# Performance work log

Measured on AMD Instinct MI355X. Metric: run time of the kernel, lower is better.

## Reference

```python
import jax, jax.numpy as jnp
import numpy as np

POOL_SIZE = 4
MAX_DIM = 256
GRID = MAX_DIM // POOL_SIZE  # 64
N_VOX = GRID ** 3            # 262144
N = 1_000_000
C = 64


def setup_inputs() -> dict:
    key = jax.random.key(0)
    k1, k2 = jax.random.split(key)
    vertices = jax.random.randint(k1, (N, 3), 0, MAX_DIM, dtype=jnp.int64)
    features = jax.random.normal(k2, (N, C), dtype=jnp.float32)
    return {"vertices": vertices, "features": features}


def reference(vertices, features):
    # floor-divide coords into voxel grid
    v = vertices // POOL_SIZE                      # [N,3] in [0, GRID)
    vox = v[:, 0] * (GRID * GRID) + v[:, 1] * GRID + v[:, 2]  # [N] flat voxel id
    # amax-pool features per voxel (empty voxels get -inf identity)
    pooled = jax.ops.segment_max(features, vox, num_segments=N_VOX)  # [N_VOX, C]
    # voxels with no points must be 0 (torch output_features initialized to zeros)
    counts = jax.ops.segment_sum(jnp.ones((vertices.shape[0],), jnp.int32), vox,
                                 num_segments=N_VOX)
    out = jnp.where((counts > 0)[:, None], pooled, jnp.zeros((), features.dtype))
    return out.reshape(-1)  # [N_VOX * C]
```

## Files before the change

kernel.cpp:

```cpp
#include <hip/hip_runtime.h>

#define GRID 64
#define N_VOX (GRID * GRID * GRID)
#define NCH 64
#define NCHUNK 256


typedef float f32x4 __attribute__((ext_vector_type(4)));
typedef int   i32x4 __attribute__((ext_vector_type(4)));

__device__ __forceinline__ int vox_of(int x, int y, int z) {
    return ((x >> 2) << 12) | ((y >> 2) << 6) | (z >> 2);
}

__device__ __forceinline__ float4 max4(float4 a, float4 b) {
    float4 r;
    r.x = fmaxf(a.x, b.x); r.y = fmaxf(a.y, b.y);
    r.z = fmaxf(a.z, b.z); r.w = fmaxf(a.w, b.w);
    return r;
}

__device__ __forceinline__ float4 ntload4(const float4* p) {
    f32x4 v = __builtin_nontemporal_load((const f32x4*)p);
    return make_float4(v[0], v[1], v[2], v[3]);
}
__device__ __forceinline__ void ntstore4(float4* p, float4 v) {
    f32x4 t; t[0] = v.x; t[1] = v.y; t[2] = v.z; t[3] = v.w;
    __builtin_nontemporal_store(t, (f32x4*)p);
}
__device__ __forceinline__ int4 ntload_i4(const int4* p) {
    i32x4 v = __builtin_nontemporal_load((const i32x4*)p);
    return make_int4(v[0], v[1], v[2], v[3]);
}

__global__ void k_hist(const int* __restrict__ verts, int* __restrict__ vox,
                       int* __restrict__ rank, int* __restrict__ counts, int n) {
    int t  = blockIdx.x * blockDim.x + threadIdx.x;
    int p0 = t * 8;
    if (p0 >= n) return;

    if (p0 + 8 <= n) {
        const int4* v4 = (const int4*)verts;
        int4 a = ntload_i4(&v4[6 * t + 0]);
        int4 b = ntload_i4(&v4[6 * t + 1]);
        int4 c = ntload_i4(&v4[6 * t + 2]);
        int4 d = ntload_i4(&v4[6 * t + 3]);
        int4 e = ntload_i4(&v4[6 * t + 4]);
        int4 f = ntload_i4(&v4[6 * t + 5]);
        int w0 = vox_of(a.x, a.y, a.z);
        int w1 = vox_of(a.w, b.x, b.y);
        int w2 = vox_of(b.z, b.w, c.x);
        int w3 = vox_of(c.y, c.z, c.w);
        int w4 = vox_of(d.x, d.y, d.z);
        int w5 = vox_of(d.w, e.x, e.y);
        int w6 = vox_of(e.z, e.w, f.x);
        int w7 = vox_of(f.y, f.z, f.w);
        ((int4*)vox)[2 * t + 0] = make_int4(w0, w1, w2, w3);
        ((int4*)vox)[2 * t + 1] = make_int4(w4, w5, w6, w7);
        int r0 = atomicAdd(&counts[w0], 1);
        int r1 = atomicAdd(&counts[w1], 1);
        int r2 = atomicAdd(&counts[w2], 1);
        int r3 = atomicAdd(&counts[w3], 1);
        int r4 = atomicAdd(&counts[w4], 1);
        int r5 = atomicAdd(&counts[w5], 1);
        int r6 = atomicAdd(&counts[w6], 1);
        int r7 = atomicAdd(&counts[w7], 1);
        ((int4*)rank)[2 * t + 0] = make_int4(r0, r1, r2, r3);
        ((int4*)rank)[2 * t + 1] = make_int4(r4, r5, r6, r7);
    } else {
        for (int p = p0; p < n; p++) {
            int w = vox_of(verts[3 * p], verts[3 * p + 1], verts[3 * p + 2]);
            vox[p]  = w;
            rank[p] = atomicAdd(&counts[w], 1);
        }
    }
}

__global__ void __launch_bounds__(256)
k_scan(const int* __restrict__ counts, int* __restrict__ gstart,
       unsigned long long* __restrict__ state, int* __restrict__ ticket) {
    __shared__ int s_ticket;
    __shared__ int wbase[4];
    __shared__ int s_base;

    if (threadIdx.x == 0) s_ticket = atomicAdd(ticket, 1);
    __syncthreads();
    const int b    = s_ticket;
    const int t    = threadIdx.x;
    const int lane = t & 63;
    const int wid  = t >> 6;

    int4 c = ((const int4*)counts)[b * 256 + t];
    int s = c.x + c.y + c.z + c.w;

    int incl = s;
    #pragma unroll
    for (int off = 1; off < 64; off <<= 1) {
        int u = __shfl_up(incl, off);
        if (lane >= off) incl += u;
    }
    if (lane == 63) wbase[wid] = incl;
    __syncthreads();

    if (wid == 0) {
        int agg = wbase[0] + wbase[1] + wbase[2] + wbase[3];
        if (lane == 0) {
            __hip_atomic_store(&state[b], (1ULL << 32) | (unsigned)agg,
                               __ATOMIC_RELEASE, __HIP_MEMORY_SCOPE_AGENT);
        }
        int excl = 0;
        int p_hi = b - 1;
        while (p_hi >= 0) {
            int p = p_hi - lane;
            unsigned long long v;
            do {
                v = (p >= 0)
                  ? __hip_atomic_load(&state[p], __ATOMIC_ACQUIRE,
                                      __HIP_MEMORY_SCOPE_AGENT)
                  : (2ULL << 32);
            } while (__any((int)((v >> 32) == 0)));
            unsigned long long m = __ballot((int)((v >> 32) == 2));
            int cut = m ? (__ffsll((long long)m) - 1) : 64;
            int contrib = (lane <= cut) ? (int)(unsigned)v : 0;
            #pragma unroll
            for (int o = 32; o; o >>= 1) contrib += __shfl_down(contrib, o);
            excl += __shfl(contrib, 0);
            if (m) break;
            p_hi -= 64;
        }
        if (lane == 0) {
            int agg2 = wbase[0] + wbase[1] + wbase[2] + wbase[3];
            __hip_atomic_store(&state[b], (2ULL << 32) | (unsigned)(excl + agg2),
                               __ATOMIC_RELEASE, __HIP_MEMORY_SCOPE_AGENT);
            s_base = excl;
            if (b == NCHUNK - 1) gstart[N_VOX] = excl + agg2;
        }
    }
    __syncthreads();

    int wexcl = 0;
    for (int i = 0; i < wid; i++) wexcl += wbase[i];
    int base = s_base + wexcl + (incl - s);
    int4 g;
    g.x = base;
    g.y = base + c.x;
    g.z = base + c.x + c.y;
    g.w = base + c.x + c.y + c.z;
    ((int4*)gstart)[b * 256 + t] = g;
}

__global__ void k_scatter_idx(const int* __restrict__ vox,
                              const int* __restrict__ rank,
                              const int* __restrict__ gstart,
                              int* __restrict__ sorted_idx, int n) {
    int t  = blockIdx.x * blockDim.x + threadIdx.x;
    int p0 = t * 8;
    if (p0 >= n) return;

    if (p0 + 8 <= n) {
        int4 w0 = ((const int4*)vox)[2 * t + 0];
        int4 w1 = ((const int4*)vox)[2 * t + 1];
        int4 r0 = ((const int4*)rank)[2 * t + 0];
        int4 r1 = ((const int4*)rank)[2 * t + 1];
        sorted_idx[gstart[w0.x] + r0.x] = p0 + 0;
        sorted_idx[gstart[w0.y] + r0.y] = p0 + 1;
        sorted_idx[gstart[w0.z] + r0.z] = p0 + 2;
        sorted_idx[gstart[w0.w] + r0.w] = p0 + 3;
        sorted_idx[gstart[w1.x] + r1.x] = p0 + 4;
        sorted_idx[gstart[w1.y] + r1.y] = p0 + 5;
        sorted_idx[gstart[w1.z] + r1.z] = p0 + 6;
        sorted_idx[gstart[w1.w] + r1.w] = p0 + 7;
    } else {
        for (int p = p0; p < n; p++)
            sorted_idx[gstart[vox[p]] + rank[p]] = p;
    }
}

#define VPB 16
#define IDX_CAP 2048

__global__ void __launch_bounds__(256)
k_gather(const int* __restrict__ sorted_idx,
         const int* __restrict__ gstart,
         const float4* __restrict__ feats4,
         float4* __restrict__ out4) {
    __shared__ int sst[VPB + 1];
    __shared__ int sidx[IDX_CAP];

    int vox0 = blockIdx.x * VPB;
    if (threadIdx.x < VPB + 1) sst[threadIdx.x] = gstart[vox0 + threadIdx.x];
    __syncthreads();

    int bstart = sst[0];
    int span   = sst[VPB] - bstart;
    bool fits  = (span <= IDX_CAP);
    if (fits) {
        for (int i = threadIdx.x; i < span; i += 256)
            sidx[i] = sorted_idx[bstart + i];
    }
    __syncthreads();

    int g   = threadIdx.x >> 4;
    int sub = threadIdx.x & 15;
    int s0  = sst[g];
    int cnt = sst[g + 1] - s0;
    float4* outp = &out4[(size_t)(vox0 + g) * 16 + sub];

    if (cnt == 0) {
        ntstore4(outp, make_float4(0.f, 0.f, 0.f, 0.f));
        return;
    }

    int off = s0 - bstart;
    float4 a0 = make_float4(-INFINITY, -INFINITY, -INFINITY, -INFINITY);
    float4 a1 = a0, a2 = a0, a3 = a0;

    int j = 0;
    for (; j + 4 <= cnt; j += 4) {
        int p0, p1, p2, p3;
        if (fits) {
            p0 = sidx[off + j];     p1 = sidx[off + j + 1];
            p2 = sidx[off + j + 2]; p3 = sidx[off + j + 3];
        } else {
            p0 = sorted_idx[s0 + j];     p1 = sorted_idx[s0 + j + 1];
            p2 = sorted_idx[s0 + j + 2]; p3 = sorted_idx[s0 + j + 3];
        }
        a0 = max4(a0, ntload4(&feats4[(size_t)p0 * 16 + sub]));
        a1 = max4(a1, ntload4(&feats4[(size_t)p1 * 16 + sub]));
        a2 = max4(a2, ntload4(&feats4[(size_t)p2 * 16 + sub]));
        a3 = max4(a3, ntload4(&feats4[(size_t)p3 * 16 + sub]));
    }
    for (; j < cnt; j++) {
        int p = fits ? sidx[off + j] : sorted_idx[s0 + j];
        a0 = max4(a0, ntload4(&feats4[(size_t)p * 16 + sub]));
    }
    ntstore4(outp, max4(max4(a0, a1), max4(a2, a3)));
}

extern "C" void kernel_launch(void* const* d_in, const int* in_sizes, int n_in,
                              void* d_out, int out_size, void* d_ws, size_t ws_size,
                              hipStream_t stream) {
    const int*   verts = (const int*)d_in[0];
    const float* feats = (const float*)d_in[1];
    float*       out   = (float*)d_out;

    const int n_pts = in_sizes[0] / 3;

    char* w = (char*)d_ws;
    int*  vox        = (int*)w;              w += (size_t)n_pts * 4;
    int*  rank       = (int*)w;              w += (size_t)n_pts * 4;
    int*  sorted_idx = (int*)w;              w += (size_t)n_pts * 4;
    int*  counts     = (int*)w;              w += (size_t)N_VOX * 4;
    unsigned long long* state = (unsigned long long*)w;  w += (size_t)NCHUNK * 8;
    int*  ticket     = (int*)w;              w += 16;
    const size_t zero_bytes = (size_t)N_VOX * 4 + (size_t)NCHUNK * 8 + 16;
    int*  gstart     = (int*)w;              w += (size_t)(N_VOX + 4) * 4;

    hipMemsetAsync(counts, 0, zero_bytes, stream);

    {
        const int block = 256;
        const int nthr  = (n_pts + 7) / 8;
        const int grid  = (nthr + block - 1) / block;
        k_hist<<<grid, block, 0, stream>>>(verts, vox, rank, counts, n_pts);
    }
    k_scan<<<NCHUNK, 256, 0, stream>>>(counts, gstart, state, ticket);

    {
        const int block = 256;
        const int nthr  = (n_pts + 7) / 8;
        const int grid  = (nthr + block - 1) / block;
        k_scatter_idx<<<grid, block, 0, stream>>>(vox, rank, gstart,
                                                  sorted_idx, n_pts);
    }
    {
        const int block = 256;
        const int grid  = N_VOX / VPB;
        k_gather<<<grid, block, 0, stream>>>(sorted_idx, gstart,
                                             (const float4*)feats, (float4*)out);
    }
}
```

Before: 433.2 us.

## Scatter features into sorted order then segment-max contiguously

Replaces the index scatter plus indirect gather with a pass that copies each point's full 256-byte feature row into voxel-sorted order, followed by a segment-max over contiguous rows. This removes the random feature reads and the sorted-index indirection from the reduction, at the cost of writing and re-reading a 256 MB intermediate buffer. The histogram kernel also drops from 8 to 4 points per thread. The scatter writes are random-position but whole-row coalesced.

```diff
diff --git a/kernel.cpp b/kernel.cpp
--- a/kernel.cpp
+++ b/kernel.cpp
@@ -36,37 +36,24 @@
 __global__ void k_hist(const int* __restrict__ verts, int* __restrict__ vox,
                        int* __restrict__ rank, int* __restrict__ counts, int n) {
     int t  = blockIdx.x * blockDim.x + threadIdx.x;
-    int p0 = t * 8;
+    int p0 = t * 4;
     if (p0 >= n) return;
 
-    if (p0 + 8 <= n) {
+    if (p0 + 4 <= n) {
         const int4* v4 = (const int4*)verts;
-        int4 a = ntload_i4(&v4[6 * t + 0]);
-        int4 b = ntload_i4(&v4[6 * t + 1]);
-        int4 c = ntload_i4(&v4[6 * t + 2]);
-        int4 d = ntload_i4(&v4[6 * t + 3]);
-        int4 e = ntload_i4(&v4[6 * t + 4]);
-        int4 f = ntload_i4(&v4[6 * t + 5]);
+        int4 a = ntload_i4(&v4[3 * t + 0]);
+        int4 b = ntload_i4(&v4[3 * t + 1]);
+        int4 c = ntload_i4(&v4[3 * t + 2]);
         int w0 = vox_of(a.x, a.y, a.z);
         int w1 = vox_of(a.w, b.x, b.y);
         int w2 = vox_of(b.z, b.w, c.x);
         int w3 = vox_of(c.y, c.z, c.w);
-        int w4 = vox_of(d.x, d.y, d.z);
-        int w5 = vox_of(d.w, e.x, e.y);
-        int w6 = vox_of(e.z, e.w, f.x);
-        int w7 = vox_of(f.y, f.z, f.w);
-        ((int4*)vox)[2 * t + 0] = make_int4(w0, w1, w2, w3);
-        ((int4*)vox)[2 * t + 1] = make_int4(w4, w5, w6, w7);
+        ((int4*)vox)[t] = make_int4(w0, w1, w2, w3);
         int r0 = atomicAdd(&counts[w0], 1);
         int r1 = atomicAdd(&counts[w1], 1);
         int r2 = atomicAdd(&counts[w2], 1);
         int r3 = atomicAdd(&counts[w3], 1);
-        int r4 = atomicAdd(&counts[w4], 1);
-        int r5 = atomicAdd(&counts[w5], 1);
-        int r6 = atomicAdd(&counts[w6], 1);
-        int r7 = atomicAdd(&counts[w7], 1);
-        ((int4*)rank)[2 * t + 0] = make_int4(r0, r1, r2, r3);
-        ((int4*)rank)[2 * t + 1] = make_int4(r4, r5, r6, r7);
+        ((int4*)rank)[t] = make_int4(r0, r1, r2, r3);
     } else {
         for (int p = p0; p < n; p++) {
             int w = vox_of(verts[3 * p], verts[3 * p + 1], verts[3 * p + 2]);
@@ -149,92 +136,52 @@
     ((int4*)gstart)[b * 256 + t] = g;
 }
 
-__global__ void k_scatter_idx(const int* __restrict__ vox,
-                              const int* __restrict__ rank,
-                              const int* __restrict__ gstart,
-                              int* __restrict__ sorted_idx, int n) {
-    int t  = blockIdx.x * blockDim.x + threadIdx.x;
-    int p0 = t * 8;
-    if (p0 >= n) return;
-
-    if (p0 + 8 <= n) {
-        int4 w0 = ((const int4*)vox)[2 * t + 0];
-        int4 w1 = ((const int4*)vox)[2 * t + 1];
-        int4 r0 = ((const int4*)rank)[2 * t + 0];
-        int4 r1 = ((const int4*)rank)[2 * t + 1];
-        sorted_idx[gstart[w0.x] + r0.x] = p0 + 0;
-        sorted_idx[gstart[w0.y] + r0.y] = p0 + 1;
-        sorted_idx[gstart[w0.z] + r0.z] = p0 + 2;
-        sorted_idx[gstart[w0.w] + r0.w] = p0 + 3;
-        sorted_idx[gstart[w1.x] + r1.x] = p0 + 4;
-        sorted_idx[gstart[w1.y] + r1.y] = p0 + 5;
-        sorted_idx[gstart[w1.z] + r1.z] = p0 + 6;
-        sorted_idx[gstart[w1.w] + r1.w] = p0 + 7;
-    } else {
-        for (int p = p0; p < n; p++)
-            sorted_idx[gstart[vox[p]] + rank[p]] = p;
-    }
-}
-
-#define VPB 16
-#define IDX_CAP 2048
-
 __global__ void __launch_bounds__(256)
-k_gather(const int* __restrict__ sorted_idx,
-         const int* __restrict__ gstart,
-         const float4* __restrict__ feats4,
-         float4* __restrict__ out4) {
-    __shared__ int sst[VPB + 1];
-    __shared__ int sidx[IDX_CAP];
-
-    int vox0 = blockIdx.x * VPB;
-    if (threadIdx.x < VPB + 1) sst[threadIdx.x] = gstart[vox0 + threadIdx.x];
-    __syncthreads();
-
-    int bstart = sst[0];
-    int span   = sst[VPB] - bstart;
-    bool fits  = (span <= IDX_CAP);
-    if (fits) {
-        for (int i = threadIdx.x; i < span; i += 256)
-            sidx[i] = sorted_idx[bstart + i];
-    }
-    __syncthreads();
-
-    int g   = threadIdx.x >> 4;
-    int sub = threadIdx.x & 15;
-    int s0  = sst[g];
-    int cnt = sst[g + 1] - s0;
-    float4* outp = &out4[(size_t)(vox0 + g) * 16 + sub];
-
-    if (cnt == 0) {
-        ntstore4(outp, make_float4(0.f, 0.f, 0.f, 0.f));
-        return;
-    }
-
-    int off = s0 - bstart;
+k_scatter_feat(const int* __restrict__ vox, const int* __restrict__ rank,
+               const int* __restrict__ gstart,
+               const float4* __restrict__ feats4,
+               float4* __restrict__ sfeat4, int n) {
+    int t   = blockIdx.x * 256 + threadIdx.x;
+    int grp = t >> 4;
+    int sub = t & 15;
+    int gw  = grp & ~3;
+    int gl  = grp & 3;
+    int pbase = gw * 4 + gl;
+
+    #pragma unroll
+    for (int i = 0; i < 4; i++) {
+        int p = pbase + i * 4;
+        if (p >= n) break;
+        float4 f = ntload4(&feats4[(size_t)p * 16 + sub]);
+        int dst = gstart[vox[p]] + rank[p];
+        sfeat4[(size_t)dst * 16 + sub] = f;
+    }
+}
+
+__global__ void __launch_bounds__(256)
+k_seg_max(const int* __restrict__ gstart,
+          const float4* __restrict__ sfeat4,
+          float4* __restrict__ out4) {
+    int t   = blockIdx.x * 256 + threadIdx.x;
+    int v   = t >> 4;
+    int sub = t & 15;
+
+    int s0 = gstart[v];
+    int s1 = gstart[v + 1];
+
     float4 a0 = make_float4(-INFINITY, -INFINITY, -INFINITY, -INFINITY);
-    float4 a1 = a0, a2 = a0, a3 = a0;
-
-    int j = 0;
-    for (; j + 4 <= cnt; j += 4) {
-        int p0, p1, p2, p3;
-        if (fits) {
-            p0 = sidx[off + j];     p1 = sidx[off + j + 1];
-            p2 = sidx[off + j + 2]; p3 = sidx[off + j + 3];
-        } else {
-            p0 = sorted_idx[s0 + j];     p1 = sorted_idx[s0 + j + 1];
-            p2 = sorted_idx[s0 + j + 2]; p3 = sorted_idx[s0 + j + 3];
-        }
-        a0 = max4(a0, ntload4(&feats4[(size_t)p0 * 16 + sub]));
-        a1 = max4(a1, ntload4(&feats4[(size_t)p1 * 16 + sub]));
-        a2 = max4(a2, ntload4(&feats4[(size_t)p2 * 16 + sub]));
-        a3 = max4(a3, ntload4(&feats4[(size_t)p3 * 16 + sub]));
-    }
-    for (; j < cnt; j++) {
-        int p = fits ? sidx[off + j] : sorted_idx[s0 + j];
-        a0 = max4(a0, ntload4(&feats4[(size_t)p * 16 + sub]));
-    }
-    ntstore4(outp, max4(max4(a0, a1), max4(a2, a3)));
+    float4 a1 = a0;
+    int s = s0;
+    for (; s + 2 <= s1; s += 2) {
+        a0 = max4(a0, sfeat4[(size_t)s       * 16 + sub]);
+        a1 = max4(a1, sfeat4[(size_t)(s + 1) * 16 + sub]);
+    }
+    if (s < s1)
+        a0 = max4(a0, sfeat4[(size_t)s * 16 + sub]);
+
+    float4 r = (s1 > s0) ? max4(a0, a1)
+                         : make_float4(0.f, 0.f, 0.f, 0.f);
+    ntstore4(&out4[(size_t)v * 16 + sub], r);
 }
 
 extern "C" void kernel_launch(void* const* d_in, const int* in_sizes, int n_in,
@@ -247,9 +194,9 @@
     const int n_pts = in_sizes[0] / 3;
 
     char* w = (char*)d_ws;
+    float4* sfeat4   = (float4*)w;           w += (size_t)n_pts * NCH * 4;
     int*  vox        = (int*)w;              w += (size_t)n_pts * 4;
     int*  rank       = (int*)w;              w += (size_t)n_pts * 4;
-    int*  sorted_idx = (int*)w;              w += (size_t)n_pts * 4;
     int*  counts     = (int*)w;              w += (size_t)N_VOX * 4;
     unsigned long long* state = (unsigned long long*)w;  w += (size_t)NCHUNK * 8;
     int*  ticket     = (int*)w;              w += 16;
@@ -260,23 +207,22 @@
 
     {
         const int block = 256;
-        const int nthr  = (n_pts + 7) / 8;
+        const int nthr  = (n_pts + 3) / 4;
         const int grid  = (nthr + block - 1) / block;
         k_hist<<<grid, block, 0, stream>>>(verts, vox, rank, counts, n_pts);
     }
     k_scan<<<NCHUNK, 256, 0, stream>>>(counts, gstart, state, ticket);
 
     {
-        const int block = 256;
-        const int nthr  = (n_pts + 7) / 8;
-        const int grid  = (nthr + block - 1) / block;
-        k_scatter_idx<<<grid, block, 0, stream>>>(vox, rank, gstart,
-                                                  sorted_idx, n_pts);
+        const int clusters = (n_pts + 15) / 16;
+        const long long threads = (long long)clusters * 64;
+        const int grid = (int)((threads + 255) / 256);
+        k_scatter_feat<<<grid, 256, 0, stream>>>(vox, rank, gstart,
+                                                 (const float4*)feats,
+                                                 sfeat4, n_pts);
     }
     {
-        const int block = 256;
-        const int grid  = N_VOX / VPB;
-        k_gather<<<grid, block, 0, stream>>>(sorted_idx, gstart,
-                                             (const float4*)feats, (float4*)out);
-    }
-}
+        const int grid = (N_VOX * 16) / 256;
+        k_seg_max<<<grid, 256, 0, stream>>>(gstart, sfeat4, (float4*)out);
+    }
+}
```

New measurement: 491.7 us. 13.5% more time.
